# Performance work log

Hardware: AMD Instinct MI355X
Metric: run time of the kernel (lower is better)

The kernel has to match this reference:

```python
import jax, jax.numpy as jnp
import numpy as np

VOCAB = 32000
HID = 2048
MAXLEN = 128


def setup_inputs() -> dict:
    key = jax.random.key(0)
    ks = jax.random.split(key, 16)
    s = 0.02
    return {
        "input_seq": jax.random.randint(ks[0], (1, 1), 0, VOCAB),
        "hidden": jax.random.normal(ks[1], (1, 1, HID), jnp.float32),
        "encoder_outputs": jax.random.normal(ks[2], (MAXLEN, HID), jnp.float32),
        "emb": jax.random.normal(ks[3], (VOCAB, HID), jnp.float32) * s,
        "attn_W": jax.random.normal(ks[4], (MAXLEN, 2 * HID), jnp.float32) * s,
        "attn_b": jnp.zeros((MAXLEN,), jnp.float32),
        "comb_W": jax.random.normal(ks[5], (HID, 2 * HID), jnp.float32) * s,
        "comb_b": jnp.zeros((HID,), jnp.float32),
        "W_ih": jax.random.normal(ks[6], (HID, HID), jnp.float32) * s,
        "W_hh": jax.random.normal(ks[7], (HID, HID), jnp.float32) * s,
        "b_ih": jnp.zeros((HID,), jnp.float32),
        "b_hh": jnp.zeros((HID,), jnp.float32),
        "out_W": jax.random.normal(ks[8], (VOCAB, HID), jnp.float32) * s,
        "out_b": jnp.zeros((VOCAB,), jnp.float32),
    }


def _rnn_step(x, h, W_ih, W_hh, b_ih, b_hh):
    # Elman RNN cell (tanh): seq_len=1 so output == new hidden. Shapes [1,1,H].
    return jnp.tanh(x @ W_ih.T + b_ih + h @ W_hh.T + b_hh)


def reference(input_seq, hidden, encoder_outputs, emb, attn_W, attn_b,
              comb_W, comb_b, W_ih, W_hh, b_ih, b_hh, out_W, out_b):
    tok = input_seq[0]                       # [1]
    x = emb[tok].reshape(1, 1, -1)           # [1,1,H]
    hidden = _rnn_step(x, hidden, W_ih, W_hh, b_ih, b_hh)   # [1,1,H]
    # second embedding of the decoder token (dropout is identity at eval)
    embedded = emb[tok].reshape(1, 1, -1)    # [1,1,H]
    attn_in = jnp.concatenate([embedded[0], hidden[0]], axis=1)   # [1,2H]
    attn_weights = jax.nn.softmax(attn_in @ attn_W.T + attn_b, axis=1)  # [1,L]
    attn_applied = attn_weights @ encoder_outputs                 # [1,H]
    o = jnp.concatenate([embedded[0], attn_applied], axis=1) @ comb_W.T + comb_b
    o = jax.nn.relu(o)[None]                 # [1,1,H]
    out_h = _rnn_step(o, hidden, W_ih, W_hh, b_ih, b_hh)          # [1,1,H]
    logits = out_h[0] @ out_W.T + out_b      # [1,VOCAB]
    return jax.nn.log_softmax(logits, axis=1)
```

## Files before the change

### kernel.cpp

```cpp
#include <hip/hip_runtime.h>
#include <hip/hip_bf16.h>
#include <math.h>

#define HID 2048
#define MAXLEN 128
#define VOCAB 32000

__device__ __forceinline__ float block_reduce_sum256(float v) {
    for (int off = 32; off > 0; off >>= 1) v += __shfl_down(v, off, 64);
    __shared__ float s[4];
    int lane = threadIdx.x & 63, w = threadIdx.x >> 6;
    if (lane == 0) s[w] = v;
    __syncthreads();
    float r = 0.f;
    if (threadIdx.x == 0) r = s[0] + s[1] + s[2] + s[3];
    return r;
}

__global__ void gather_row_kernel(const float* __restrict__ emb,
                                  const int* __restrict__ tok,
                                  float* __restrict__ x) {
    int i = blockIdx.x * blockDim.x + threadIdx.x;
    if (i < HID) x[i] = emb[(size_t)tok[0] * HID + i];
}

__global__ void dual_matvec_kernel(const float* __restrict__ W1, const float* __restrict__ x1,
                                   const float* __restrict__ W2, const float* __restrict__ x2,
                                   const float* __restrict__ b1, const float* __restrict__ b2,
                                   float* __restrict__ out, int act) {
    int r = blockIdx.x;
    const float4* w1 = (const float4*)(W1 + (size_t)r * HID);
    const float4* w2 = (const float4*)(W2 + (size_t)r * HID);
    const float4* v1 = (const float4*)x1;
    const float4* v2 = (const float4*)x2;
    const int K4 = HID / 4;
    float p = 0.f;
    for (int i = threadIdx.x; i < K4; i += blockDim.x) {
        float4 a = w1[i], b = v1[i];
        p += a.x * b.x + a.y * b.y + a.z * b.z + a.w * b.w;
        float4 c = w2[i], d = v2[i];
        p += c.x * d.x + c.y * d.y + c.z * d.z + c.w * d.w;
    }
    float s = block_reduce_sum256(p);
    if (threadIdx.x == 0) {
        s += b1[r] + b2[r];
        if (act == 1) s = tanhf(s);
        else if (act == 2) s = fmaxf(s, 0.f);
        out[r] = s;
    }
}

__global__ void concat_matvec_kernel(const float* __restrict__ W,
                                     const float* __restrict__ xa, const float* __restrict__ xb,
                                     const float* __restrict__ bias,
                                     float* __restrict__ out, int act) {
    int r = blockIdx.x;
    const float4* w = (const float4*)(W + (size_t)r * (2 * HID));
    const float4* va = (const float4*)xa;
    const float4* vb = (const float4*)xb;
    const int K4 = HID / 4;
    float p = 0.f;
    for (int i = threadIdx.x; i < K4; i += blockDim.x) {
        float4 a = w[i], b = va[i];
        p += a.x * b.x + a.y * b.y + a.z * b.z + a.w * b.w;
        float4 c = w[i + K4], d = vb[i];
        p += c.x * d.x + c.y * d.y + c.z * d.z + c.w * d.w;
    }
    float s = block_reduce_sum256(p);
    if (threadIdx.x == 0) {
        s += bias[r];
        if (act == 1) s = tanhf(s);
        else if (act == 2) s = fmaxf(s, 0.f);
        out[r] = s;
    }
}

__global__ void softmax128_kernel(float* __restrict__ logits) {
    int t = threadIdx.x;
    float a = logits[t], b = logits[t + 64];
    float m = fmaxf(a, b);
    for (int off = 32; off > 0; off >>= 1) m = fmaxf(m, __shfl_xor(m, off, 64));
    float ea = expf(a - m), eb = expf(b - m);
    float s = ea + eb;
    for (int off = 32; off > 0; off >>= 1) s += __shfl_xor(s, off, 64);
    logits[t] = ea / s;
    logits[t + 64] = eb / s;
}

__global__ void attn_apply_kernel(const float* __restrict__ wts,
                                  const float* __restrict__ enc,
                                  float* __restrict__ out) {
    int j = blockIdx.x * blockDim.x + threadIdx.x;
    if (j >= HID) return;
    float acc = 0.f;
    for (int l = 0; l < MAXLEN; ++l) acc += wts[l] * enc[(size_t)l * HID + j];
    out[j] = acc;
}

__global__ void matvec_kernel(const float* __restrict__ W, const float* __restrict__ x,
                              const float* __restrict__ bias, float* __restrict__ out) {
    int r = blockIdx.x;
    const float4* w = (const float4*)(W + (size_t)r * HID);
    const float4* v = (const float4*)x;
    const int K4 = HID / 4;
    float p = 0.f;
    for (int i = threadIdx.x; i < K4; i += blockDim.x) {
        float4 a = w[i], b = v[i];
        p += a.x * b.x + a.y * b.y + a.z * b.z + a.w * b.w;
    }
    float s = block_reduce_sum256(p);
    if (threadIdx.x == 0) out[r] = s + bias[r];
}

__global__ void log_softmax_kernel(float* __restrict__ io, int n) {
    __shared__ float red[16];
    const int t = threadIdx.x;
    const int lane = t & 63, w = t >> 6;
    float m = -INFINITY;
    for (int i = t; i < n; i += 1024) m = fmaxf(m, io[i]);
    for (int off = 32; off > 0; off >>= 1) m = fmaxf(m, __shfl_xor(m, off, 64));
    if (lane == 0) red[w] = m;
    __syncthreads();
    float bm = red[0];
    for (int i = 1; i < 16; ++i) bm = fmaxf(bm, red[i]);
    __syncthreads();
    float s = 0.f;
    for (int i = t; i < n; i += 1024) s += expf(io[i] - bm);
    for (int off = 32; off > 0; off >>= 1) s += __shfl_xor(s, off, 64);
    if (lane == 0) red[w] = s;
    __syncthreads();
    float bs = 0.f;
    for (int i = 0; i < 16; ++i) bs += red[i];
    float lg = bm + logf(bs);
    __syncthreads();
    for (int i = t; i < n; i += 1024) io[i] -= lg;
}

extern "C" void kernel_launch(void* const* d_in, const int* in_sizes, int n_in,
                              void* d_out, int out_size, void* d_ws, size_t ws_size,
                              hipStream_t stream) {
    const int*   tok    = (const int*)  d_in[0];
    const float* hidden = (const float*)d_in[1];
    const float* enc    = (const float*)d_in[2];
    const float* emb    = (const float*)d_in[3];
    const float* attn_W = (const float*)d_in[4];
    const float* attn_b = (const float*)d_in[5];
    const float* comb_W = (const float*)d_in[6];
    const float* comb_b = (const float*)d_in[7];
    const float* W_ih   = (const float*)d_in[8];
    const float* W_hh   = (const float*)d_in[9];
    const float* b_ih   = (const float*)d_in[10];
    const float* b_hh   = (const float*)d_in[11];
    const float* out_W  = (const float*)d_in[12];
    const float* out_b  = (const float*)d_in[13];
    float* out = (float*)d_out;

    float* ws = (float*)d_ws;
    float* X  = ws;
    float* H1 = ws + 2048;
    float* AL = ws + 4096;
    float* AA = ws + 6144;
    float* O  = ws + 8192;
    float* OH = ws + 10240;

    gather_row_kernel<<<HID / 256, 256, 0, stream>>>(emb, tok, X);
    dual_matvec_kernel<<<HID, 256, 0, stream>>>(W_ih, X, W_hh, hidden, b_ih, b_hh, H1, 1);
    concat_matvec_kernel<<<MAXLEN, 256, 0, stream>>>(attn_W, X, H1, attn_b, AL, 0);
    softmax128_kernel<<<1, 64, 0, stream>>>(AL);
    attn_apply_kernel<<<HID / 256, 256, 0, stream>>>(AL, enc, AA);
    concat_matvec_kernel<<<HID, 256, 0, stream>>>(comb_W, X, AA, comb_b, O, 2);
    dual_matvec_kernel<<<HID, 256, 0, stream>>>(W_ih, O, W_hh, H1, b_ih, b_hh, OH, 1);
    matvec_kernel<<<VOCAB, 256, 0, stream>>>(out_W, OH, out_b, out);
    log_softmax_kernel<<<1, 1024, 0, stream>>>(out, VOCAB);
}
```

Baseline: 97.34 us.

## Use one wave per row for matvecs and fuse the gather, softmax and log-softmax steps

```diff
diff --git a/kernel.cpp b/kernel.cpp
--- a/kernel.cpp
+++ b/kernel.cpp
@@ -1,139 +1,116 @@
 #include <hip/hip_runtime.h>
-#include <hip/hip_bf16.h>
 #include <math.h>
 
 #define HID 2048
+#define KQ (HID / 4)
 #define MAXLEN 128
 #define VOCAB 32000
 
-__device__ __forceinline__ float block_reduce_sum256(float v) {
-    for (int off = 32; off > 0; off >>= 1) v += __shfl_down(v, off, 64);
-    __shared__ float s[4];
-    int lane = threadIdx.x & 63, w = threadIdx.x >> 6;
-    if (lane == 0) s[w] = v;
-    __syncthreads();
-    float r = 0.f;
-    if (threadIdx.x == 0) r = s[0] + s[1] + s[2] + s[3];
-    return r;
+__device__ __forceinline__ float wave_sum(float v) {
+    #pragma unroll
+    for (int m = 1; m < 64; m <<= 1) v += __shfl_xor(v, m, 64);
+    return v;
 }
 
-__global__ void gather_row_kernel(const float* __restrict__ emb,
-                                  const int* __restrict__ tok,
-                                  float* __restrict__ x) {
-    int i = blockIdx.x * blockDim.x + threadIdx.x;
-    if (i < HID) x[i] = emb[(size_t)tok[0] * HID + i];
+__device__ __forceinline__ float dot4(const float4 a, const float4 b) {
+    return a.x * b.x + a.y * b.y + a.z * b.z + a.w * b.w;
 }
 
-__global__ void dual_matvec_kernel(const float* __restrict__ W1, const float* __restrict__ x1,
-                                   const float* __restrict__ W2, const float* __restrict__ x2,
-                                   const float* __restrict__ b1, const float* __restrict__ b2,
-                                   float* __restrict__ out, int act) {
-    int r = blockIdx.x;
+__global__ void rnn_cell_kernel(const float* __restrict__ W1, const float* __restrict__ x1,
+                                const int* __restrict__ tok,
+                                const float* __restrict__ W2, const float* __restrict__ x2,
+                                const float* __restrict__ b1, const float* __restrict__ b2,
+                                float* __restrict__ out) {
+    const int r = blockIdx.x * 4 + (threadIdx.x >> 6);
+    const int lane = threadIdx.x & 63;
+    const float4* xa = (const float4*)(tok ? x1 + (size_t)tok[0] * HID : x1);
+    const float4* xb = (const float4*)x2;
     const float4* w1 = (const float4*)(W1 + (size_t)r * HID);
     const float4* w2 = (const float4*)(W2 + (size_t)r * HID);
-    const float4* v1 = (const float4*)x1;
-    const float4* v2 = (const float4*)x2;
-    const int K4 = HID / 4;
     float p = 0.f;
-    for (int i = threadIdx.x; i < K4; i += blockDim.x) {
-        float4 a = w1[i], b = v1[i];
-        p += a.x * b.x + a.y * b.y + a.z * b.z + a.w * b.w;
-        float4 c = w2[i], d = v2[i];
-        p += c.x * d.x + c.y * d.y + c.z * d.z + c.w * d.w;
+    #pragma unroll 8
+    for (int i = lane; i < KQ; i += 64) {
+        p += dot4(w1[i], xa[i]);
+        p += dot4(w2[i], xb[i]);
     }
-    float s = block_reduce_sum256(p);
-    if (threadIdx.x == 0) {
-        s += b1[r] + b2[r];
-        if (act == 1) s = tanhf(s);
-        else if (act == 2) s = fmaxf(s, 0.f);
-        out[r] = s;
+    p = wave_sum(p);
+    if (lane == 0) out[r] = tanhf(p + b1[r] + b2[r]);
+}
+
+template<int ACT>
+__global__ void concat_mv_kernel(const float* __restrict__ W,
+                                 const float* __restrict__ emb, const int* __restrict__ tok,
+                                 const float* __restrict__ xb,
+                                 const float* __restrict__ b,
+                                 float* __restrict__ out) {
+    const int r = blockIdx.x * 4 + (threadIdx.x >> 6);
+    const int lane = threadIdx.x & 63;
+    const float4* xa = (const float4*)(emb + (size_t)tok[0] * HID);
+    const float4* xv = (const float4*)xb;
+    const float4* w  = (const float4*)(W + (size_t)r * 2 * HID);
+    float p = 0.f;
+    #pragma unroll 8
+    for (int i = lane; i < KQ; i += 64) {
+        p += dot4(w[i], xa[i]);
+        p += dot4(w[i + KQ], xv[i]);
+    }
+    p = wave_sum(p);
+    if (lane == 0) {
+        p += b[r];
+        if (ACT == 2) p = fmaxf(p, 0.f);
+        out[r] = p;
     }
 }
 
-__global__ void concat_matvec_kernel(const float* __restrict__ W,
-                                     const float* __restrict__ xa, const float* __restrict__ xb,
-                                     const float* __restrict__ bias,
-                                     float* __restrict__ out, int act) {
-    int r = blockIdx.x;
-    const float4* w = (const float4*)(W + (size_t)r * (2 * HID));
-    const float4* va = (const float4*)xa;
-    const float4* vb = (const float4*)xb;
-    const int K4 = HID / 4;
-    float p = 0.f;
-    for (int i = threadIdx.x; i < K4; i += blockDim.x) {
-        float4 a = w[i], b = va[i];
-        p += a.x * b.x + a.y * b.y + a.z * b.z + a.w * b.w;
-        float4 c = w[i + K4], d = vb[i];
-        p += c.x * d.x + c.y * d.y + c.z * d.z + c.w * d.w;
-    }
-    float s = block_reduce_sum256(p);
-    if (threadIdx.x == 0) {
-        s += bias[r];
-        if (act == 1) s = tanhf(s);
-        else if (act == 2) s = fmaxf(s, 0.f);
-        out[r] = s;
-    }
-}
-
-__global__ void softmax128_kernel(float* __restrict__ logits) {
-    int t = threadIdx.x;
-    float a = logits[t], b = logits[t + 64];
-    float m = fmaxf(a, b);
-    for (int off = 32; off > 0; off >>= 1) m = fmaxf(m, __shfl_xor(m, off, 64));
-    float ea = expf(a - m), eb = expf(b - m);
-    float s = ea + eb;
-    for (int off = 32; off > 0; off >>= 1) s += __shfl_xor(s, off, 64);
-    logits[t] = ea / s;
-    logits[t + 64] = eb / s;
-}
-
-__global__ void attn_apply_kernel(const float* __restrict__ wts,
-                                  const float* __restrict__ enc,
-                                  float* __restrict__ out) {
-    int j = blockIdx.x * blockDim.x + threadIdx.x;
-    if (j >= HID) return;
+__global__ void softmax_apply_kernel(const float* __restrict__ AL,
+                                     const float* __restrict__ enc,
+                                     float* __restrict__ out) {
+    __shared__ float sAL[MAXLEN];
+    __shared__ float wts[MAXLEN];
+    const int t = threadIdx.x;
+    if (t < MAXLEN) sAL[t] = AL[t];
+    __syncthreads();
+    float m = sAL[0];
+    for (int l = 1; l < MAXLEN; ++l) m = fmaxf(m, sAL[l]);
+    float s = 0.f;
+    for (int l = 0; l < MAXLEN; ++l) s += expf(sAL[l] - m);
+    if (t < MAXLEN) wts[t] = expf(sAL[t] - m) / s;
+    __syncthreads();
+    const int j = blockIdx.x * blockDim.x + t;
     float acc = 0.f;
+    #pragma unroll 4
     for (int l = 0; l < MAXLEN; ++l) acc += wts[l] * enc[(size_t)l * HID + j];
     out[j] = acc;
 }
 
-__global__ void matvec_kernel(const float* __restrict__ W, const float* __restrict__ x,
-                              const float* __restrict__ bias, float* __restrict__ out) {
-    int r = blockIdx.x;
-    const float4* w = (const float4*)(W + (size_t)r * HID);
-    const float4* v = (const float4*)x;
-    const int K4 = HID / 4;
+__global__ void bigmv_kernel(const float* __restrict__ W, const float* __restrict__ x,
+                             const float* __restrict__ b, float* __restrict__ out,
+                             float* __restrict__ partial) {
+    const int r = blockIdx.x * 4 + (threadIdx.x >> 6);
+    const int lane = threadIdx.x & 63;
+    const float4* xv = (const float4*)x;
+    const float4* w  = (const float4*)(W + (size_t)r * HID);
     float p = 0.f;
-    for (int i = threadIdx.x; i < K4; i += blockDim.x) {
-        float4 a = w[i], b = v[i];
-        p += a.x * b.x + a.y * b.y + a.z * b.z + a.w * b.w;
+    #pragma unroll 8
+    for (int i = lane; i < KQ; i += 64) p += dot4(w[i], xv[i]);
+    p = wave_sum(p);
+    if (lane == 0) {
+        p += b[r];
+        out[r] = p;
+        atomicAdd(&partial[r & 255], expf(p));
     }
-    float s = block_reduce_sum256(p);
-    if (threadIdx.x == 0) out[r] = s + bias[r];
 }
 
-__global__ void log_softmax_kernel(float* __restrict__ io, int n) {
-    __shared__ float red[16];
-    const int t = threadIdx.x;
-    const int lane = t & 63, w = t >> 6;
-    float m = -INFINITY;
-    for (int i = t; i < n; i += 1024) m = fmaxf(m, io[i]);
-    for (int off = 32; off > 0; off >>= 1) m = fmaxf(m, __shfl_xor(m, off, 64));
-    if (lane == 0) red[w] = m;
+__global__ void finalize_kernel(const float* __restrict__ partial, float* __restrict__ out) {
+    __shared__ float red[4];
+    const int t = threadIdx.x, lane = t & 63, w = t >> 6;
+    float v = partial[t];
+    v = wave_sum(v);
+    if (lane == 0) red[w] = v;
     __syncthreads();
-    float bm = red[0];
-    for (int i = 1; i < 16; ++i) bm = fmaxf(bm, red[i]);
-    __syncthreads();
-    float s = 0.f;
-    for (int i = t; i < n; i += 1024) s += expf(io[i] - bm);
-    for (int off = 32; off > 0; off >>= 1) s += __shfl_xor(s, off, 64);
-    if (lane == 0) red[w] = s;
-    __syncthreads();
-    float bs = 0.f;
-    for (int i = 0; i < 16; ++i) bs += red[i];
-    float lg = bm + logf(bs);
-    __syncthreads();
-    for (int i = t; i < n; i += 1024) io[i] -= lg;
+    const float lg = logf(red[0] + red[1] + red[2] + red[3]);
+    const int i = blockIdx.x * 256 + t;
+    out[i] -= lg;
 }
 
 extern "C" void kernel_launch(void* const* d_in, const int* in_sizes, int n_in,
@@ -156,20 +133,19 @@
     float* out = (float*)d_out;
 
     float* ws = (float*)d_ws;
-    float* X  = ws;
-    float* H1 = ws + 2048;
-    float* AL = ws + 4096;
-    float* AA = ws + 6144;
-    float* O  = ws + 8192;
-    float* OH = ws + 10240;
+    float* H1 = ws;
+    float* AL = ws + 2048;
+    float* AA = ws + 2176;
+    float* O  = ws + 4224;
+    float* OH = ws + 6272;
+    float* P  = ws + 8320;
 
-    gather_row_kernel<<<HID / 256, 256, 0, stream>>>(emb, tok, X);
-    dual_matvec_kernel<<<HID, 256, 0, stream>>>(W_ih, X, W_hh, hidden, b_ih, b_hh, H1, 1);
-    concat_matvec_kernel<<<MAXLEN, 256, 0, stream>>>(attn_W, X, H1, attn_b, AL, 0);
-    softmax128_kernel<<<1, 64, 0, stream>>>(AL);
-    attn_apply_kernel<<<HID / 256, 256, 0, stream>>>(AL, enc, AA);
-    concat_matvec_kernel<<<HID, 256, 0, stream>>>(comb_W, X, AA, comb_b, O, 2);
-    dual_matvec_kernel<<<HID, 256, 0, stream>>>(W_ih, O, W_hh, H1, b_ih, b_hh, OH, 1);
-    matvec_kernel<<<VOCAB, 256, 0, stream>>>(out_W, OH, out_b, out);
-    log_softmax_kernel<<<1, 1024, 0, stream>>>(out, VOCAB);
+    rnn_cell_kernel<<<HID / 4, 256, 0, stream>>>(W_ih, emb, tok, W_hh, hidden, b_ih, b_hh, H1);
+    concat_mv_kernel<0><<<MAXLEN / 4, 256, 0, stream>>>(attn_W, emb, tok, H1, attn_b, AL);
+    softmax_apply_kernel<<<HID / 256, 256, 0, stream>>>(AL, enc, AA);
+    concat_mv_kernel<2><<<HID / 4, 256, 0, stream>>>(comb_W, emb, tok, AA, comb_b, O);
+    rnn_cell_kernel<<<HID / 4, 256, 0, stream>>>(W_ih, O, nullptr, W_hh, H1, b_ih, b_hh, OH);
+    hipMemsetAsync(P, 0, 256 * sizeof(float), stream);
+    bigmv_kernel<<<VOCAB / 4, 256, 0, stream>>>(out_W, OH, out_b, out, P);
+    finalize_kernel<<<VOCAB / 256, 256, 0, stream>>>(P, out);
 }
```

Measured after the change: 113.6 us. +16.8%, slower.
